# Kernel tuning notes

Hardware: AMD Instinct MI355X
Metric: run time of the kernel (lower is better)

Reference implementation:

```python
import jax, jax.numpy as jnp
import numpy as np

CHEB_K = 3

def avwgcn(x, E, W_pool, b_pool):
    # x: [B,N,Cin], E: [N,e], W_pool: [e,K,Cin,Cout], b_pool: [e,Cout]
    N = E.shape[0]
    A = jax.nn.softmax(jax.nn.relu(E @ E.T), axis=1)          # adaptive adjacency [N,N]
    supports = [jnp.eye(N, dtype=x.dtype), A]
    for _ in range(2, CHEB_K):
        supports.append(2.0 * (A @ supports[-1]) - supports[-2])
    S = jnp.stack(supports)                                    # [K,N,N]
    W = jnp.einsum('ne,ekio->nkio', E, W_pool)                 # per-node weights
    b = E @ b_pool                                             # [N,Cout]
    xg = jnp.einsum('knm,bmi->bnki', S, x)                     # Chebyshev graph conv
    return jnp.einsum('bnki,nkio->bno', xg, W) + b


def setup_inputs() -> dict:
    key = jax.random.key(0)
    ks = jax.random.split(key, 7)
    B, N, Din, Dout, E_DIM = 64, 1024, 64, 64, 16
    C = Din + Dout
    return {
        'x': jax.random.normal(ks[0], (B, N, Din), dtype=jnp.float32),
        'state': jax.random.normal(ks[1], (B, N, Dout), dtype=jnp.float32),
        'node_embeddings': jax.random.normal(ks[2], (N, E_DIM), dtype=jnp.float32),
        'gate_W_pool': jax.random.normal(ks[3], (E_DIM, CHEB_K, C, 2 * Dout), dtype=jnp.float32) * 0.1,
        'gate_b_pool': jax.random.normal(ks[4], (E_DIM, 2 * Dout), dtype=jnp.float32) * 0.1,
        'upd_W_pool': jax.random.normal(ks[5], (E_DIM, CHEB_K, C, Dout), dtype=jnp.float32) * 0.1,
        'upd_b_pool': jax.random.normal(ks[6], (E_DIM, Dout), dtype=jnp.float32) * 0.1,
    }


def reference(x, state, node_embeddings, gate_W_pool, gate_b_pool, upd_W_pool, upd_b_pool):
    hidden_dim = state.shape[-1]
    input_and_state = jnp.concatenate([x, state], axis=-1)
    z_r = jax.nn.sigmoid(avwgcn(input_and_state, node_embeddings, gate_W_pool, gate_b_pool))
    z, r = z_r[..., :hidden_dim], z_r[..., hidden_dim:]
    candidate = jnp.concatenate([x, z * state], axis=-1)
    hc = jnp.tanh(avwgcn(candidate, node_embeddings, upd_W_pool, upd_b_pool))
    return r * state + (1.0 - r) * hc
```

## Files before the change

### kernel.cpp

```cpp
#include <hip/hip_runtime.h>
#include <math.h>

#define N_NODES 1024
#define B_SZ 64
#define GNH 4096
#define KI 384
#define EDIM 16

typedef _Float16 half8_t __attribute__((ext_vector_type(8)));
typedef float f32x4 __attribute__((ext_vector_type(4)));

__device__ __forceinline__ unsigned short f2h(float f) {
    _Float16 h = (_Float16)f;
    return *(unsigned short*)&h;
}
__device__ __forceinline__ float h2f(unsigned short u) {
    _Float16 h = *(_Float16*)&u;
    return (float)h;
}
__device__ __forceinline__ float sigmoidf_(float v) {
    return 1.f / (1.f + __expf(-v));
}
__device__ __forceinline__ void load_lds16(const void* g, void* l) {
    __builtin_amdgcn_global_load_lds(
        (const __attribute__((address_space(1))) void*)g,
        (__attribute__((address_space(3))) void*)l, 16, 0, 0);
}

__global__ __launch_bounds__(256) void compute_A_kernel(
    const float* __restrict__ E, unsigned short* __restrict__ Ah) {
    __shared__ float red[256];
    const int tid = threadIdx.x;
    const int n = blockIdx.x;
    float en[EDIM];
#pragma unroll
    for (int e = 0; e < EDIM; ++e) en[e] = E[n * EDIM + e];
    float logit[4], lmax = -1e30f;
#pragma unroll
    for (int j = 0; j < 4; ++j) {
        const int m = tid + j * 256;
        float d = 0.f;
#pragma unroll
        for (int e = 0; e < EDIM; ++e) d += en[e] * E[m * EDIM + e];
        d = fmaxf(d, 0.f);
        logit[j] = d;
        lmax = fmaxf(lmax, d);
    }
    red[tid] = lmax;
    __syncthreads();
    for (int s = 128; s > 0; s >>= 1) {
        if (tid < s) red[tid] = fmaxf(red[tid], red[tid + s]);
        __syncthreads();
    }
    lmax = red[0];
    __syncthreads();
    float ex[4], lsum = 0.f;
#pragma unroll
    for (int j = 0; j < 4; ++j) {
        ex[j] = __expf(logit[j] - lmax);
        lsum += ex[j];
    }
    red[tid] = lsum;
    __syncthreads();
    for (int s = 128; s > 0; s >>= 1) {
        if (tid < s) red[tid] += red[tid + s];
        __syncthreads();
    }
    const float inv = 1.f / red[0];
#pragma unroll
    for (int j = 0; j < 4; ++j)
        Ah[n * N_NODES + tid + j * 256] = f2h(ex[j] * inv);
}

__global__ __launch_bounds__(256) void build_T0_kernel(
    const float* __restrict__ x, const float* __restrict__ state,
    unsigned short* __restrict__ TX0, unsigned short* __restrict__ TS0) {
    const int n = blockIdx.x;
    const int tid = threadIdx.x;
#pragma unroll
    for (int t = 0; t < 32; ++t) {
        const int idx = t * 256 + tid;
        const int c = idx & 127;
        const int b = idx >> 7;
        if (c < 64)
            TX0[(size_t)n * GNH + b * 64 + c] =
                f2h(x[((size_t)b * N_NODES + n) * 64 + c]);
        else
            TS0[(size_t)n * GNH + b * 64 + (c - 64)] =
                f2h(state[((size_t)b * N_NODES + n) * 64 + (c - 64)]);
    }
}

__global__ __launch_bounds__(256) void transpose16_kernel(
    const unsigned short* __restrict__ src, unsigned short* __restrict__ dst,
    int W) {
    __shared__ unsigned short Ls[64 * 72];
    const int tid = threadIdx.x;
    const int r0 = blockIdx.x * 64;
    const int c0 = blockIdx.y * 64;
#pragma unroll
    for (int t = 0; t < 2; ++t) {
        const int id = t * 256 + tid;
        const int row = id >> 3;
        const int c8 = id & 7;
        uint4 v = *(const uint4*)&src[(size_t)(r0 + row) * W + c0 + c8 * 8];
        const unsigned short* vp = (const unsigned short*)&v;
#pragma unroll
        for (int j = 0; j < 8; ++j) Ls[(c8 * 8 + j) * 72 + row] = vp[j];
    }
    __syncthreads();
#pragma unroll
    for (int t = 0; t < 2; ++t) {
        const int id = t * 256 + tid;
        const int c = id >> 3;
        const int r8 = id & 7;
        uint4 v = *(const uint4*)&Ls[c * 72 + r8 * 8];
        *(uint4*)&dst[(size_t)(c0 + c) * N_NODES + r0 + r8 * 8] = v;
    }
}

__global__ __launch_bounds__(256) void gemm_s2_kernel(
    const unsigned short* __restrict__ Ah,
    const unsigned short* __restrict__ AhT, unsigned short* __restrict__ S2h) {
    __shared__ unsigned short As[64 * 64];
    __shared__ unsigned short Bs[64 * 64];
    const int tid = threadIdx.x;
    const int wave = tid >> 6;
    const int lane = tid & 63;
    const int l15 = lane & 15;
    const int quad = lane >> 4;
    const int n0 = blockIdx.x * 64;
    const int m0 = blockIdx.y * 64;
    const int wn = wave * 16;
    const int lr = lane >> 3;
    const int lsw = (lane & 7) ^ lr;

    f32x4 acc[4] = {};
    for (int k0 = 0; k0 < N_NODES; k0 += 64) {
#pragma unroll
        for (int i = 0; i < 2; ++i) {
            const int rbase = (wave * 2 + i) * 8;
            load_lds16(&Ah[(size_t)(n0 + rbase + lr) * N_NODES + k0 + lsw * 8],
                       &As[rbase * 64]);
            load_lds16(&AhT[(size_t)(m0 + rbase + lr) * N_NODES + k0 + lsw * 8],
                       &Bs[rbase * 64]);
        }
        __syncthreads();
#pragma unroll
        for (int ks = 0; ks < 2; ++ks) {
            const int slot = ((ks * 4 + quad) ^ (l15 & 7)) * 8;
            const half8_t b = *(const half8_t*)&Bs[(wn + l15) * 64 + slot];
#pragma unroll
            for (int mi = 0; mi < 4; ++mi) {
                const half8_t a = *(const half8_t*)&As[(mi * 16 + l15) * 64 + slot];
                acc[mi] =
                    __builtin_amdgcn_mfma_f32_16x16x32_f16(a, b, acc[mi], 0, 0, 0);
            }
        }
        __syncthreads();
    }
#pragma unroll
    for (int mi = 0; mi < 4; ++mi) {
#pragma unroll
        for (int r = 0; r < 4; ++r) {
            const int n_g = n0 + mi * 16 + quad * 4 + r;
            const int m_g = m0 + wn + l15;
            const float v = 2.f * acc[mi][r] - (n_g == m_g ? 1.f : 0.f);
            S2h[(size_t)n_g * N_NODES + m_g] = f2h(v);
        }
    }
}

__global__ __launch_bounds__(256) void gemm_graph_kernel(
    const unsigned short* __restrict__ Ah,
    const unsigned short* __restrict__ S2h,
    const unsigned short* __restrict__ BTX,
    const unsigned short* __restrict__ BTS,
    unsigned short* __restrict__ T1X, unsigned short* __restrict__ T1S,
    unsigned short* __restrict__ T2X, unsigned short* __restrict__ T2S,
    int ysplit) {
    __shared__ union {
        struct {
            unsigned short As[128 * 64];
            unsigned short Bs[128 * 64];
        } s;
        unsigned short Cs[64 * 136];
    } lds;
    const int tid = threadIdx.x;
    const int wave = tid >> 6;
    const int lane = tid & 63;
    const int l15 = lane & 15;
    const int quad = lane >> 4;
    const int wm = (wave >> 1) * 64;
    const int wn = (wave & 1) * 64;
    const int mrow0 = blockIdx.x * 128;
    const bool isA = mrow0 < N_NODES;
    const unsigned short* Asrc =
        (isA ? Ah : S2h) + (size_t)(mrow0 & 1023) * N_NODES;
    const bool isX = (int)blockIdx.y < ysplit;
    const int col0 = (isX ? blockIdx.y : blockIdx.y - ysplit) * 128;
    const unsigned short* Bsrc =
        (isX ? BTX : BTS) + (size_t)col0 * N_NODES;
    unsigned short* OUT =
        (isA ? (isX ? T1X : T1S) : (isX ? T2X : T2S)) +
        (size_t)(mrow0 & 1023) * GNH + col0;
    const int lr = lane >> 3;
    const int lsw = (lane & 7) ^ lr;

    f32x4 acc[4][4] = {};

    for (int k0 = 0; k0 < N_NODES; k0 += 64) {
#pragma unroll
        for (int i = 0; i < 4; ++i) {
            const int rbase = (wave * 4 + i) * 8;
            load_lds16(&Asrc[(size_t)(rbase + lr) * N_NODES + k0 + lsw * 8],
                       &lds.s.As[rbase * 64]);
        }
#pragma unroll
        for (int i = 0; i < 4; ++i) {
            const int rbase = (wave * 4 + i) * 8;
            load_lds16(&Bsrc[(size_t)(rbase + lr) * N_NODES + k0 + lsw * 8],
                       &lds.s.Bs[rbase * 64]);
        }
        __syncthreads();
#pragma unroll
        for (int ks = 0; ks < 2; ++ks) {
            const int slot = ((ks * 4 + quad) ^ (l15 & 7)) * 8;
            half8_t a[4], b[4];
#pragma unroll
            for (int mi = 0; mi < 4; ++mi)
                a[mi] = *(const half8_t*)&lds.s
                             .As[(wm + mi * 16 + l15) * 64 + slot];
#pragma unroll
            for (int ni = 0; ni < 4; ++ni)
                b[ni] = *(const half8_t*)&lds.s
                             .Bs[(wn + ni * 16 + l15) * 64 + slot];
#pragma unroll
            for (int mi = 0; mi < 4; ++mi)
#pragma unroll
                for (int ni = 0; ni < 4; ++ni)
                    acc[mi][ni] = __builtin_amdgcn_mfma_f32_16x16x32_f16(
                        a[mi], b[ni], acc[mi][ni], 0, 0, 0);
        }
        __syncthreads();
    }

#pragma unroll
    for (int p = 0; p < 2; ++p) {
        if (p) __syncthreads();
        if ((wave >> 1) == p) {
#pragma unroll
            for (int mi = 0; mi < 4; ++mi)
#pragma unroll
                for (int ni = 0; ni < 4; ++ni)
#pragma unroll
                    for (int r = 0; r < 4; ++r) {
                        const int row = mi * 16 + quad * 4 + r;
                        const int col = wn + ni * 16 + l15;
                        lds.Cs[row * 136 + col] = f2h(acc[mi][ni][r]);
                    }
        }
        __syncthreads();
#pragma unroll
        for (int i = 0; i < 4; ++i) {
            const int id = i * 256 + tid;
            const int row = id >> 4;
            const int c8 = id & 15;
            uint4 cv = *(const uint4*)&lds.Cs[row * 136 + c8 * 8];
            *(uint4*)&OUT[(size_t)(p * 64 + row) * GNH + c8 * 8] = cv;
        }
    }
}

__global__ __launch_bounds__(256) void dequant_kernel(
    const float* __restrict__ Wp, const float* __restrict__ E,
    unsigned short* __restrict__ Wt, int NO) {
    __shared__ float En[32 * 16];
    const int tid = threadIdx.x;
    const int ki0 = blockIdx.x * 32;
    const int o0 = blockIdx.y * 32;
    const int n0 = blockIdx.z * 32;
    const int o = tid >> 3;
    const int k4 = tid & 7;

#pragma unroll
    for (int t = 0; t < 2; ++t) {
        const int id = t * 256 + tid;
        En[id] = E[(n0 + (id >> 4)) * EDIM + (id & 15)];
    }
    __syncthreads();

    f32x4 w[EDIM];
#pragma unroll
    for (int e = 0; e < EDIM; ++e) {
        f32x4 v;
#pragma unroll
        for (int j = 0; j < 4; ++j)
            v[j] = Wp[(size_t)(e * KI + ki0 + k4 * 4 + j) * NO + o0 + o];
        w[e] = v;
    }

    const size_t wt_base = ((size_t)n0 * NO + (o0 + o)) * KI + ki0 + k4 * 4;
#pragma unroll 4
    for (int nl = 0; nl < 32; ++nl) {
        f32x4 a = {0.f, 0.f, 0.f, 0.f};
#pragma unroll
        for (int e = 0; e < EDIM; ++e) a += w[e] * En[nl * EDIM + e];
        union { unsigned short u[4]; uint2 v; } pk;
#pragma unroll
        for (int j = 0; j < 4; ++j) pk.u[j] = f2h(a[j]);
        *(uint2*)&Wt[wt_base + (size_t)nl * NO * KI] = pk.v;
    }
}

__global__ __launch_bounds__(256) void pernode_gate_kernel(
    const unsigned short* __restrict__ TX0,
    const unsigned short* __restrict__ TS0,
    const unsigned short* __restrict__ TX1,
    const unsigned short* __restrict__ TS1,
    const unsigned short* __restrict__ TX2,
    const unsigned short* __restrict__ TS2,
    const unsigned short* __restrict__ Wt, const float* __restrict__ E,
    const float* __restrict__ bp, const float* __restrict__ state,
    float* __restrict__ rbuf, unsigned short* __restrict__ ts0_out) {
    __shared__ unsigned short XsX[64 * 64];
    __shared__ unsigned short XsS[64 * 64];
    const int n = blockIdx.x;
    const int tid = threadIdx.x;
    const int wave = tid >> 6;
    const int lane = tid & 63;
    const int l15 = lane & 15;
    const int quad = lane >> 4;
    const int wn = wave * 32;
    const int lr = lane >> 3;
    const int lsw = (lane & 7) ^ lr;

    float bias[2];
#pragma unroll
    for (int ni = 0; ni < 2; ++ni) {
        float bv = 0.f;
#pragma unroll
        for (int e = 0; e < EDIM; ++e)
            bv += E[n * EDIM + e] * bp[e * 128 + wn + ni * 16 + l15];
        bias[ni] = bv;
    }

    f32x4 acc[4][2] = {};

    const unsigned short* TXs[3] = {TX0, TX1, TX2};
    const unsigned short* TSs[3] = {TS0, TS1, TS2};
    const unsigned short* wrow0 = Wt + ((size_t)n * 128 + wn + l15) * KI;
    const unsigned short* wrow1 = Wt + ((size_t)n * 128 + wn + 16 + l15) * KI;

    for (int s = 0; s < 3; ++s) {
        const unsigned short* xs = TXs[s] + (size_t)n * GNH;
        const unsigned short* ss = TSs[s] + (size_t)n * GNH;
#pragma unroll
        for (int i = 0; i < 2; ++i) {
            const int slab = wave * 2 + i;
            load_lds16(xs + (slab * 8 + lr) * 64 + lsw * 8, &XsX[slab * 512]);
            load_lds16(ss + (slab * 8 + lr) * 64 + lsw * 8, &XsS[slab * 512]);
        }
        __syncthreads();
#pragma unroll
        for (int ks = 0; ks < 4; ++ks) {
            const int kseg = ks * 4 + quad;
            half8_t b[2];
            b[0] = *(const half8_t*)&wrow0[s * 128 + kseg * 8];
            b[1] = *(const half8_t*)&wrow1[s * 128 + kseg * 8];
            const unsigned short* plane = (kseg < 8) ? XsX : XsS;
            const int aslot = ((kseg & 7) ^ (l15 & 7)) * 8;
#pragma unroll
            for (int mi = 0; mi < 4; ++mi) {
                const half8_t a =
                    *(const half8_t*)&plane[(mi * 16 + l15) * 64 + aslot];
#pragma unroll
                for (int ni = 0; ni < 2; ++ni)
                    acc[mi][ni] = __builtin_amdgcn_mfma_f32_16x16x32_f16(
                        a, b[ni], acc[mi][ni], 0, 0, 0);
            }
        }
        __syncthreads();
    }

#pragma unroll
    for (int mi = 0; mi < 4; ++mi) {
#pragma unroll
        for (int r = 0; r < 4; ++r) {
            const int b_g = mi * 16 + quad * 4 + r;
#pragma unroll
            for (int ni = 0; ni < 2; ++ni) {
                const int o_g = wn + ni * 16 + l15;
                const float v = sigmoidf_(acc[mi][ni][r] + bias[ni]);
                if (o_g < 64) {
                    const float sv =
                        state[((size_t)b_g * N_NODES + n) * 64 + o_g];
                    ts0_out[(size_t)n * GNH + b_g * 64 + o_g] = f2h(v * sv);
                } else {
                    rbuf[((size_t)n * B_SZ + b_g) * 64 + (o_g - 64)] = v;
                }
            }
        }
    }
}

__global__ __launch_bounds__(256) void pernode_upd_kernel(
    const unsigned short* __restrict__ TX0,
    const unsigned short* __restrict__ TS0,
    const unsigned short* __restrict__ TX1,
    const unsigned short* __restrict__ TS1,
    const unsigned short* __restrict__ TX2,
    const unsigned short* __restrict__ TS2,
    const unsigned short* __restrict__ Wt, const float* __restrict__ E,
    const float* __restrict__ bp, const float* __restrict__ state,
    const float* __restrict__ rbuf, float* __restrict__ out) {
    __shared__ unsigned short XsX[64 * 64];
    __shared__ unsigned short XsS[64 * 64];
    const int n = blockIdx.x;
    const int tid = threadIdx.x;
    const int wave = tid >> 6;
    const int lane = tid & 63;
    const int l15 = lane & 15;
    const int quad = lane >> 4;
    const int wn = wave * 16;
    const int o_g = wn + l15;
    const int lr = lane >> 3;
    const int lsw = (lane & 7) ^ lr;

    float bias = 0.f;
#pragma unroll
    for (int e = 0; e < EDIM; ++e)
        bias += E[n * EDIM + e] * bp[e * 64 + o_g];

    f32x4 acc[4] = {};

    const unsigned short* TXs[3] = {TX0, TX1, TX2};
    const unsigned short* TSs[3] = {TS0, TS1, TS2};
    const unsigned short* wrow = Wt + ((size_t)n * 64 + o_g) * KI;

    for (int s = 0; s < 3; ++s) {
        const unsigned short* xs = TXs[s] + (size_t)n * GNH;
        const unsigned short* ss = TSs[s] + (size_t)n * GNH;
#pragma unroll
        for (int i = 0; i < 2; ++i) {
            const int slab = wave * 2 + i;
            load_lds16(xs + (slab * 8 + lr) * 64 + lsw * 8, &XsX[slab * 512]);
            load_lds16(ss + (slab * 8 + lr) * 64 + lsw * 8, &XsS[slab * 512]);
        }
        __syncthreads();
#pragma unroll
        for (int ks = 0; ks < 4; ++ks) {
            const int kseg = ks * 4 + quad;
            const half8_t b = *(const half8_t*)&wrow[s * 128 + kseg * 8];
            const unsigned short* plane = (kseg < 8) ? XsX : XsS;
            const int aslot = ((kseg & 7) ^ (l15 & 7)) * 8;
#pragma unroll
            for (int mi = 0; mi < 4; ++mi) {
                const half8_t a =
                    *(const half8_t*)&plane[(mi * 16 + l15) * 64 + aslot];
                acc[mi] = __builtin_amdgcn_mfma_f32_16x16x32_f16(a, b, acc[mi],
                                                                 0, 0, 0);
            }
        }
        __syncthreads();
    }

#pragma unroll
    for (int mi = 0; mi < 4; ++mi) {
#pragma unroll
        for (int r = 0; r < 4; ++r) {
            const int b_g = mi * 16 + quad * 4 + r;
            const float hc = tanhf(acc[mi][r] + bias);
            const float rr = rbuf[((size_t)n * B_SZ + b_g) * 64 + o_g];
            const float sv = state[((size_t)b_g * N_NODES + n) * 64 + o_g];
            out[((size_t)b_g * N_NODES + n) * 64 + o_g] =
                rr * sv + (1.f - rr) * hc;
        }
    }
}

extern "C" void kernel_launch(void* const* d_in, const int* in_sizes, int n_in,
                              void* d_out, int out_size, void* d_ws,
                              size_t ws_size, hipStream_t stream) {
    const float* x = (const float*)d_in[0];
    const float* state = (const float*)d_in[1];
    const float* E = (const float*)d_in[2];
    const float* gW = (const float*)d_in[3];
    const float* gb = (const float*)d_in[4];
    const float* uW = (const float*)d_in[5];
    const float* ub = (const float*)d_in[6];
    float* out = (float*)d_out;

    char* ws = (char*)d_ws;
    unsigned short* Ah = (unsigned short*)ws;
    unsigned short* AhT = (unsigned short*)(ws + 2097152);
    unsigned short* S2h = (unsigned short*)(ws + 4194304);
    unsigned short* TX0 = (unsigned short*)(ws + 6291456);
    unsigned short* TS0 = (unsigned short*)(ws + 14680064);
    unsigned short* TX0T = (unsigned short*)(ws + 23068672);
    unsigned short* TS0T = (unsigned short*)(ws + 31457280);
    unsigned short* TX1 = (unsigned short*)(ws + 39845888);
    unsigned short* TS1 = (unsigned short*)(ws + 48234496);
    unsigned short* TX2 = (unsigned short*)(ws + 56623104);
    unsigned short* TS2 = (unsigned short*)(ws + 65011712);
    unsigned short* Wt = (unsigned short*)(ws + 73400320);
    float* rbuf = (float*)(ws + 174063616);

    compute_A_kernel<<<N_NODES, 256, 0, stream>>>(E, Ah);
    build_T0_kernel<<<N_NODES, 256, 0, stream>>>(x, state, TX0, TS0);
    transpose16_kernel<<<dim3(16, 16), 256, 0, stream>>>(Ah, AhT, N_NODES);
    transpose16_kernel<<<dim3(16, 64), 256, 0, stream>>>(TX0, TX0T, GNH);
    transpose16_kernel<<<dim3(16, 64), 256, 0, stream>>>(TS0, TS0T, GNH);
    gemm_s2_kernel<<<dim3(16, 16), 256, 0, stream>>>(Ah, AhT, S2h);

    gemm_graph_kernel<<<dim3(16, 64), 256, 0, stream>>>(
        Ah, S2h, TX0T, TS0T, TX1, TS1, TX2, TS2, 32);
    dequant_kernel<<<dim3(12, 4, 32), 256, 0, stream>>>(gW, E, Wt, 128);
    pernode_gate_kernel<<<N_NODES, 256, 0, stream>>>(
        TX0, TS0, TX1, TS1, TX2, TS2, Wt, E, gb, state, rbuf, TS0);
    transpose16_kernel<<<dim3(16, 64), 256, 0, stream>>>(TS0, TS0T, GNH);

    gemm_graph_kernel<<<dim3(16, 32), 256, 0, stream>>>(
        Ah, S2h, TX0T, TS0T, TX1, TS1, TX2, TS2, 0);
    dequant_kernel<<<dim3(12, 2, 32), 256, 0, stream>>>(uW, E, Wt, 64);
    pernode_upd_kernel<<<N_NODES, 256, 0, stream>>>(
        TX0, TS0, TX1, TS1, TX2, TS2, Wt, E, ub, state, rbuf, out);
}
```

Baseline: 327.2 us.

## Fuse T0 build with transposes, XCD-aware graph GEMM tiling, fp16 r buffer

The fp16 conversion of x and state now also writes the transposed copies through LDS in the same kernel, which removes two separate transpose launches and their re-reads of TX0/TS0. The graph GEMM uses a 1D grid whose block index is remapped so that each XCD handles a contiguous set of column tiles, aiming to improve L2 reuse of the B operand. The r gate buffer is stored in fp16 instead of fp32 to halve that traffic, at the cost of some precision in r. The fused build kernel's reads are still coalesced per batch slice, but its scattered 2-byte stores to TX0 may be less efficient than before.

```diff
diff --git a/kernel.cpp b/kernel.cpp
--- a/kernel.cpp
+++ b/kernel.cpp
@@ -72,22 +72,38 @@
         Ah[n * N_NODES + tid + j * 256] = f2h(ex[j] * inv);
 }
 
-__global__ __launch_bounds__(256) void build_T0_kernel(
+__global__ __launch_bounds__(256) void build_T0_all_kernel(
     const float* __restrict__ x, const float* __restrict__ state,
-    unsigned short* __restrict__ TX0, unsigned short* __restrict__ TS0) {
-    const int n = blockIdx.x;
-    const int tid = threadIdx.x;
-#pragma unroll
-    for (int t = 0; t < 32; ++t) {
-        const int idx = t * 256 + tid;
-        const int c = idx & 127;
-        const int b = idx >> 7;
-        if (c < 64)
-            TX0[(size_t)n * GNH + b * 64 + c] =
-                f2h(x[((size_t)b * N_NODES + n) * 64 + c]);
-        else
-            TS0[(size_t)n * GNH + b * 64 + (c - 64)] =
-                f2h(state[((size_t)b * N_NODES + n) * 64 + (c - 64)]);
+    unsigned short* __restrict__ TX0, unsigned short* __restrict__ TS0,
+    unsigned short* __restrict__ TX0T, unsigned short* __restrict__ TS0T) {
+    __shared__ unsigned short Lx[64 * 72];
+    __shared__ unsigned short Lss[64 * 72];
+    const int tid = threadIdx.x;
+    const int n0 = blockIdx.x * 64;
+    const int b = blockIdx.y;
+#pragma unroll
+    for (int t = 0; t < 16; ++t) {
+        const int id = t * 256 + tid;
+        const int nl = id >> 6;
+        const int c = id & 63;
+        const float xv = x[((size_t)b * N_NODES + n0 + nl) * 64 + c];
+        const float sv = state[((size_t)b * N_NODES + n0 + nl) * 64 + c];
+        const unsigned short xh = f2h(xv), sh = f2h(sv);
+        TX0[(size_t)(n0 + nl) * GNH + b * 64 + c] = xh;
+        TS0[(size_t)(n0 + nl) * GNH + b * 64 + c] = sh;
+        Lx[c * 72 + nl] = xh;
+        Lss[c * 72 + nl] = sh;
+    }
+    __syncthreads();
+#pragma unroll
+    for (int t = 0; t < 2; ++t) {
+        const int id = t * 256 + tid;
+        const int c = id >> 3;
+        const int n8 = id & 7;
+        uint4 xv = *(const uint4*)&Lx[c * 72 + n8 * 8];
+        uint4 sv = *(const uint4*)&Lss[c * 72 + n8 * 8];
+        *(uint4*)&TX0T[(size_t)(b * 64 + c) * N_NODES + n0 + n8 * 8] = xv;
+        *(uint4*)&TS0T[(size_t)(b * 64 + c) * N_NODES + n0 + n8 * 8] = sv;
     }
 }
 
@@ -178,7 +194,7 @@
     const unsigned short* __restrict__ BTS,
     unsigned short* __restrict__ T1X, unsigned short* __restrict__ T1S,
     unsigned short* __restrict__ T2X, unsigned short* __restrict__ T2S,
-    int ysplit) {
+    int ysplit, int colsPerXcd) {
     __shared__ union {
         struct {
             unsigned short As[128 * 64];
@@ -193,12 +209,16 @@
     const int quad = lane >> 4;
     const int wm = (wave >> 1) * 64;
     const int wn = (wave & 1) * 64;
-    const int mrow0 = blockIdx.x * 128;
+    const int id = blockIdx.x;
+    const int xcd = id & 7;
+    const int j = id >> 3;
+    const int mrow0 = (j & 15) * 128;
+    const int ytile = xcd * colsPerXcd + (j >> 4);
     const bool isA = mrow0 < N_NODES;
     const unsigned short* Asrc =
         (isA ? Ah : S2h) + (size_t)(mrow0 & 1023) * N_NODES;
-    const bool isX = (int)blockIdx.y < ysplit;
-    const int col0 = (isX ? blockIdx.y : blockIdx.y - ysplit) * 128;
+    const bool isX = ytile < ysplit;
+    const int col0 = (isX ? ytile : ytile - ysplit) * 128;
     const unsigned short* Bsrc =
         (isX ? BTX : BTS) + (size_t)col0 * N_NODES;
     unsigned short* OUT =
@@ -263,9 +283,9 @@
         __syncthreads();
 #pragma unroll
         for (int i = 0; i < 4; ++i) {
-            const int id = i * 256 + tid;
-            const int row = id >> 4;
-            const int c8 = id & 15;
+            const int id2 = i * 256 + tid;
+            const int row = id2 >> 4;
+            const int c8 = id2 & 15;
             uint4 cv = *(const uint4*)&lds.Cs[row * 136 + c8 * 8];
             *(uint4*)&OUT[(size_t)(p * 64 + row) * GNH + c8 * 8] = cv;
         }
@@ -322,7 +342,7 @@
     const unsigned short* __restrict__ TS2,
     const unsigned short* __restrict__ Wt, const float* __restrict__ E,
     const float* __restrict__ bp, const float* __restrict__ state,
-    float* __restrict__ rbuf, unsigned short* __restrict__ ts0_out) {
+    unsigned short* __restrict__ rbuf, unsigned short* __restrict__ ts0_out) {
     __shared__ unsigned short XsX[64 * 64];
     __shared__ unsigned short XsS[64 * 64];
     const int n = blockIdx.x;
@@ -397,7 +417,7 @@
                         state[((size_t)b_g * N_NODES + n) * 64 + o_g];
                     ts0_out[(size_t)n * GNH + b_g * 64 + o_g] = f2h(v * sv);
                 } else {
-                    rbuf[((size_t)n * B_SZ + b_g) * 64 + (o_g - 64)] = v;
+                    rbuf[((size_t)n * B_SZ + b_g) * 64 + (o_g - 64)] = f2h(v);
                 }
             }
         }
@@ -413,7 +433,7 @@
     const unsigned short* __restrict__ TS2,
     const unsigned short* __restrict__ Wt, const float* __restrict__ E,
     const float* __restrict__ bp, const float* __restrict__ state,
-    const float* __restrict__ rbuf, float* __restrict__ out) {
+    const unsigned short* __restrict__ rbuf, float* __restrict__ out) {
     __shared__ unsigned short XsX[64 * 64];
     __shared__ unsigned short XsS[64 * 64];
     const int n = blockIdx.x;
@@ -471,7 +491,7 @@
         for (int r = 0; r < 4; ++r) {
             const int b_g = mi * 16 + quad * 4 + r;
             const float hc = tanhf(acc[mi][r] + bias);
-            const float rr = rbuf[((size_t)n * B_SZ + b_g) * 64 + o_g];
+            const float rr = h2f(rbuf[((size_t)n * B_SZ + b_g) * 64 + o_g]);
             const float sv = state[((size_t)b_g * N_NODES + n) * 64 + o_g];
             out[((size_t)b_g * N_NODES + n) * 64 + o_g] =
                 rr * sv + (1.f - rr) * hc;
@@ -504,24 +524,23 @@
     unsigned short* TX2 = (unsigned short*)(ws + 56623104);
     unsigned short* TS2 = (unsigned short*)(ws + 65011712);
     unsigned short* Wt = (unsigned short*)(ws + 73400320);
-    float* rbuf = (float*)(ws + 174063616);
+    unsigned short* rbuf = (unsigned short*)(ws + 174063616);
 
     compute_A_kernel<<<N_NODES, 256, 0, stream>>>(E, Ah);
-    build_T0_kernel<<<N_NODES, 256, 0, stream>>>(x, state, TX0, TS0);
+    build_T0_all_kernel<<<dim3(16, 64), 256, 0, stream>>>(x, state, TX0, TS0,
+                                                          TX0T, TS0T);
     transpose16_kernel<<<dim3(16, 16), 256, 0, stream>>>(Ah, AhT, N_NODES);
-    transpose16_kernel<<<dim3(16, 64), 256, 0, stream>>>(TX0, TX0T, GNH);
-    transpose16_kernel<<<dim3(16, 64), 256, 0, stream>>>(TS0, TS0T, GNH);
     gemm_s2_kernel<<<dim3(16, 16), 256, 0, stream>>>(Ah, AhT, S2h);
 
-    gemm_graph_kernel<<<dim3(16, 64), 256, 0, stream>>>(
-        Ah, S2h, TX0T, TS0T, TX1, TS1, TX2, TS2, 32);
+    gemm_graph_kernel<<<1024, 256, 0, stream>>>(
+        Ah, S2h, TX0T, TS0T, TX1, TS1, TX2, TS2, 32, 8);
     dequant_kernel<<<dim3(12, 4, 32), 256, 0, stream>>>(gW, E, Wt, 128);
     pernode_gate_kernel<<<N_NODES, 256, 0, stream>>>(
         TX0, TS0, TX1, TS1, TX2, TS2, Wt, E, gb, state, rbuf, TS0);
     transpose16_kernel<<<dim3(16, 64), 256, 0, stream>>>(TS0, TS0T, GNH);
 
-    gemm_graph_kernel<<<dim3(16, 32), 256, 0, stream>>>(
-        Ah, S2h, TX0T, TS0T, TX1, TS1, TX2, TS2, 0);
+    gemm_graph_kernel<<<512, 256, 0, stream>>>(
+        Ah, S2h, TX0T, TS0T, TX1, TS1, TX2, TS2, 0, 4);
     dequant_kernel<<<dim3(12, 2, 32), 256, 0, stream>>>(uW, E, Wt, 64);
     pernode_upd_kernel<<<N_NODES, 256, 0, stream>>>(
         TX0, TS0, TX1, TS1, TX2, TS2, Wt, E, ub, state, rbuf, out);
```

Measured after the change: 307.8 us (median of 2 runs). 1.06x faster.
